# Performance work log

Hardware: AMD Instinct MI355X
Metric: run time of the kernel (lower is better)

The kernel has to match this reference:

```python
import jax, jax.numpy as jnp
import numpy as np

EPS = 1e-10
TWO_PI = 2.0 * np.pi


def _nll(y_target, o_pred):
    # getCoef: split last dim of o_pred into 5 bivariate-Gaussian params
    mux = o_pred[..., 0]
    muy = o_pred[..., 1]
    sx = jnp.exp(o_pred[..., 2])
    sy = jnp.exp(o_pred[..., 3])
    corr = jnp.tanh(o_pred[..., 4])

    norm_x = (y_target[..., 1] - mux) / sx
    norm_y = (y_target[..., 2] - muy) / sy
    z = norm_x ** 2 + norm_y ** 2 - 2.0 * corr * norm_x * norm_y
    onemrho = 1.0 - corr ** 2
    top = jnp.exp(-z / (2.0 * onemrho))
    bottom = TWO_PI * (sx * sy * jnp.sqrt(onemrho))
    pdf = top / bottom  # (B, T, P)

    # sum over all (b, t, p) of -log(clamp(pdf, eps)), divided by ped_num
    total = jnp.sum(-jnp.log(jnp.clip(pdf, EPS)))
    return total / pdf.shape[2]


def setup_inputs() -> dict:
    key = jax.random.key(0)
    k1, k2 = jax.random.split(key)
    B, T, P = 64, 128, 512
    y_target = jax.random.normal(k1, (B, T, P, 3), dtype=jnp.float32)
    o_pred = jax.random.normal(k2, (B, T, P, 5), dtype=jnp.float32)
    return {"y_target": y_target, "o_pred": o_pred}


def reference(y_target, o_pred):
    return _nll(y_target, o_pred)
```

## Files before the change

### kernel.cpp

```cpp
#include <hip/hip_runtime.h>
#include <hip/hip_bf16.h>


#define THREADS 256
#define PPT 4
#define TILE (THREADS * PPT)
#define MAXBLOCKS 512

typedef float v4 __attribute__((ext_vector_type(4)));
typedef __attribute__((address_space(3))) v4 as3_v4;
typedef const __attribute__((address_space(1))) v4 as1_v4;

__device__ __forceinline__ float point_nll(float mux, float muy, float lsx,
                                           float lsy, float w, float y1, float y2) {
    const float LOG_2PI = 1.8378770664093453f;
    const float CLIP    = 23.025850929940457f;
    float isx  = __expf(-lsx);
    float isy  = __expf(-lsy);
    float nx   = (y1 - mux) * isx;
    float ny   = (y2 - muy) * isy;
    float e2w  = __expf(2.0f * w);
    float corr = fmaf(-2.0f, __builtin_amdgcn_rcpf(e2w + 1.0f), 1.0f);
    float omr  = fmaf(-corr, corr, 1.0f);
    float z    = fmaf(nx, nx, ny * ny) - 2.0f * corr * nx * ny;
    float nll  = fmaf(z, 0.5f * __builtin_amdgcn_rcpf(omr),
                      fmaf(0.5f, __logf(omr), lsx + lsy + LOG_2PI));
    return fminf(nll, CLIP);
}

__global__ __launch_bounds__(THREADS) void nll_partial_kernel(
    const float* __restrict__ y, const float* __restrict__ o,
    float* __restrict__ partial, int N) {
    __shared__ v4 lds[4][2][512];
    const int tid  = threadIdx.x;
    const int wave = tid >> 6;
    const int lane = tid & 63;
    const v4* o4 = (const v4*)o;
    const v4* y4 = (const v4*)y;

    const int nfull = N / TILE;
    const int step  = gridDim.x;
    float acc = 0.0f;

    auto issue = [&](int t, int b) {
        const v4* gob = o4 + (long long)t * 1280 + wave * 320 + lane;
        const v4* gyb = y4 + (long long)t * 768  + wave * 192 + lane;
        v4* ob = &lds[wave][b][0];
        v4* yb = &lds[wave][b][320];
#pragma unroll
        for (int k = 0; k < 5; ++k)
            __builtin_amdgcn_global_load_lds((as1_v4*)(gob + k * 64),
                                             (as3_v4*)(ob + k * 64), 16, 0, 2 );
#pragma unroll
        for (int k = 0; k < 3; ++k)
            __builtin_amdgcn_global_load_lds((as1_v4*)(gyb + k * 64),
                                             (as3_v4*)(yb + k * 64), 16, 0, 2 );
    };

    int t = blockIdx.x;
    int p = 0;
    if (t < nfull) issue(t, p);
    while (t < nfull) {
        const int  tn  = t + step;
        const bool pre = tn < nfull;
        if (pre) issue(tn, p ^ 1);

        if (pre) __builtin_amdgcn_s_waitcnt(0x0F78);
        else     __builtin_amdgcn_s_waitcnt(0x0F70);
        asm volatile("" ::: "memory");

        const float* fo = (const float*)&lds[wave][p][0]   + lane * (PPT * 5);
        const float* fy = (const float*)&lds[wave][p][320] + lane * (PPT * 3);
#pragma unroll
        for (int j = 0; j < PPT; ++j) {
            acc += point_nll(fo[5 * j + 0], fo[5 * j + 1], fo[5 * j + 2],
                             fo[5 * j + 3], fo[5 * j + 4],
                             fy[3 * j + 1], fy[3 * j + 2]);
        }
        p ^= 1;
        t = tn;
    }

    long long gid = (long long)blockIdx.x * THREADS + tid;
    for (long long i = (long long)nfull * TILE + gid; i < (long long)N;
         i += (long long)step * THREADS) {
        acc += point_nll(o[i * 5 + 0], o[i * 5 + 1], o[i * 5 + 2],
                         o[i * 5 + 3], o[i * 5 + 4],
                         y[i * 3 + 1], y[i * 3 + 2]);
    }

#pragma unroll
    for (int off = 32; off > 0; off >>= 1) acc += __shfl_down(acc, off, 64);
    __shared__ float ws[THREADS / 64];
    if (lane == 0) ws[wave] = acc;
    __syncthreads();
    if (tid == 0) {
        float s = 0.0f;
#pragma unroll
        for (int i = 0; i < THREADS / 64; ++i) s += ws[i];
        partial[blockIdx.x] = s;
    }
}

__global__ __launch_bounds__(THREADS) void nll_final_kernel(
    const float* __restrict__ partial, int nparts, float* __restrict__ out,
    float inv_p) {
    float acc = 0.0f;
    for (int i = threadIdx.x; i < nparts; i += THREADS) acc += partial[i];
#pragma unroll
    for (int off = 32; off > 0; off >>= 1) acc += __shfl_down(acc, off, 64);
    __shared__ float ws[THREADS / 64];
    if ((threadIdx.x & 63) == 0) ws[threadIdx.x >> 6] = acc;
    __syncthreads();
    if (threadIdx.x == 0) {
        float s = 0.0f;
#pragma unroll
        for (int i = 0; i < THREADS / 64; ++i) s += ws[i];
        out[0] = s * inv_p;
    }
}

extern "C" void kernel_launch(void* const* d_in, const int* in_sizes, int n_in,
                              void* d_out, int out_size, void* d_ws, size_t ws_size,
                              hipStream_t stream) {
    const float* y = (const float*)d_in[0];
    const float* o = (const float*)d_in[1];
    int N = in_sizes[1] / 5;
    int ntiles = (N + TILE - 1) / TILE;
    int blocks = ntiles < MAXBLOCKS ? ntiles : MAXBLOCKS;
    if (blocks < 1) blocks = 1;

    float* partial = (float*)d_ws;
    nll_partial_kernel<<<blocks, THREADS, 0, stream>>>(y, o, partial, N);
    nll_final_kernel<<<1, THREADS, 0, stream>>>(partial, blocks, (float*)d_out,
                                                1.0f / 512.0f);
}
```

Before: 150.0 us.

## Load targets into registers, shrink LDS tiles, double grid size for occupancy

The y_target stream now goes straight into registers with per-thread vector loads, so only o_pred is staged through LDS with async global-to-LDS copies. This cuts the LDS footprint per block from 64KB to 40KB. Together with a launch-bounds hint of 4 blocks per CU and a doubled grid cap, more blocks can be resident per CU to hide memory latency. The main loop is unrolled by two so each LDS buffer pairs with its own set of y registers. The cost is higher register pressure. The existing vmcnt-based waits still rely on the same count of 8 outstanding loads per tile.

```diff
diff --git a/kernel.cpp b/kernel.cpp
--- a/kernel.cpp
+++ b/kernel.cpp
@@ -5,7 +5,7 @@
 #define THREADS 256
 #define PPT 4
 #define TILE (THREADS * PPT)
-#define MAXBLOCKS 512
+#define MAXBLOCKS 1024
 
 typedef float v4 __attribute__((ext_vector_type(4)));
 typedef __attribute__((address_space(3))) v4 as3_v4;
@@ -28,10 +28,10 @@
     return fminf(nll, CLIP);
 }
 
-__global__ __launch_bounds__(THREADS) void nll_partial_kernel(
+__global__ __launch_bounds__(THREADS, 4) void nll_partial_kernel(
     const float* __restrict__ y, const float* __restrict__ o,
     float* __restrict__ partial, int N) {
-    __shared__ v4 lds[4][2][512];
+    __shared__ v4 lds[4][2][320];
     const int tid  = threadIdx.x;
     const int wave = tid >> 6;
     const int lane = tid & 63;
@@ -42,43 +42,49 @@
     const int step  = gridDim.x;
     float acc = 0.0f;
 
-    auto issue = [&](int t, int b) {
+    auto issue_o = [&](int t, int b) {
         const v4* gob = o4 + (long long)t * 1280 + wave * 320 + lane;
-        const v4* gyb = y4 + (long long)t * 768  + wave * 192 + lane;
         v4* ob = &lds[wave][b][0];
-        v4* yb = &lds[wave][b][320];
 #pragma unroll
         for (int k = 0; k < 5; ++k)
             __builtin_amdgcn_global_load_lds((as1_v4*)(gob + k * 64),
                                              (as3_v4*)(ob + k * 64), 16, 0, 2 );
-#pragma unroll
-        for (int k = 0; k < 3; ++k)
-            __builtin_amdgcn_global_load_lds((as1_v4*)(gyb + k * 64),
-                                             (as3_v4*)(yb + k * 64), 16, 0, 2 );
+    };
+    auto load_y = [&](int t, v4& z0, v4& z1, v4& z2) {
+        const v4* gy = y4 + (long long)t * 768 + wave * 192 + lane * 3;
+        z0 = gy[0]; z1 = gy[1]; z2 = gy[2];
+    };
+    auto wait_cur = [&](bool pre) {
+        if (pre) __builtin_amdgcn_s_waitcnt(0x0F78);
+        else     __builtin_amdgcn_s_waitcnt(0x0F70);
+        asm volatile("" ::: "memory");
+    };
+    auto compute = [&](int b, v4 z0, v4 z1, v4 z2) {
+        const float* fo = (const float*)&lds[wave][b][0] + lane * (PPT * 5);
+        acc += point_nll(fo[0],  fo[1],  fo[2],  fo[3],  fo[4],  z0[1], z0[2]);
+        acc += point_nll(fo[5],  fo[6],  fo[7],  fo[8],  fo[9],  z1[0], z1[1]);
+        acc += point_nll(fo[10], fo[11], fo[12], fo[13], fo[14], z1[3], z2[0]);
+        acc += point_nll(fo[15], fo[16], fo[17], fo[18], fo[19], z2[2], z2[3]);
     };
 
     int t = blockIdx.x;
-    int p = 0;
-    if (t < nfull) issue(t, p);
+    v4 ya0, ya1, ya2, yb0, yb1, yb2;
+    if (t < nfull) { issue_o(t, 0); load_y(t, ya0, ya1, ya2); }
     while (t < nfull) {
-        const int  tn  = t + step;
-        const bool pre = tn < nfull;
-        if (pre) issue(tn, p ^ 1);
+        const int  t1   = t + step;
+        const bool pre1 = t1 < nfull;
+        if (pre1) { issue_o(t1, 1); load_y(t1, yb0, yb1, yb2); }
+        wait_cur(pre1);
+        compute(0, ya0, ya1, ya2);
+        if (!pre1) break;
 
-        if (pre) __builtin_amdgcn_s_waitcnt(0x0F78);
-        else     __builtin_amdgcn_s_waitcnt(0x0F70);
-        asm volatile("" ::: "memory");
-
-        const float* fo = (const float*)&lds[wave][p][0]   + lane * (PPT * 5);
-        const float* fy = (const float*)&lds[wave][p][320] + lane * (PPT * 3);
-#pragma unroll
-        for (int j = 0; j < PPT; ++j) {
-            acc += point_nll(fo[5 * j + 0], fo[5 * j + 1], fo[5 * j + 2],
-                             fo[5 * j + 3], fo[5 * j + 4],
-                             fy[3 * j + 1], fy[3 * j + 2]);
-        }
-        p ^= 1;
-        t = tn;
+        const int  t2   = t1 + step;
+        const bool pre2 = t2 < nfull;
+        if (pre2) { issue_o(t2, 0); load_y(t2, ya0, ya1, ya2); }
+        wait_cur(pre2);
+        compute(1, yb0, yb1, yb2);
+        if (!pre2) break;
+        t = t2;
     }
 
     long long gid = (long long)blockIdx.x * THREADS + tid;
```

Result: slower. 157.7 us (+5.1%).
